# Kernel tuning notes

Measured on AMD Instinct MI355X. Metric: run time of the kernel, lower is better.

Reference implementation:

```python
import jax, jax.numpy as jnp
import numpy as np

DELTA = 0.1
B, U_DIM, D_DIM, H_DIM, Y_DIM = 4096, 256, 64, 8192, 256
ORDER = H_DIM // 2  # 2x2 rotation blocks


def setup_inputs() -> dict:
    key = jax.random.key(0)
    k = jax.random.split(key, 6)
    u = jax.random.normal(k[0], (B, U_DIM), jnp.float32)
    du = jax.random.normal(k[1], (B, D_DIM), jnp.float32)
    h = jax.random.normal(k[2], (1, H_DIM), jnp.float32)          # h_init state
    # torch.nn.init.uniform_ -> U[0,1); +0.05 keeps 1/omega well-conditioned
    omega = jax.random.uniform(k[3], (ORDER,), jnp.float32) + 0.05
    B_w = jax.random.normal(k[4], (H_DIM, U_DIM + D_DIM), jnp.float32) / np.sqrt(U_DIM + D_DIM)
    C_w = jax.random.normal(k[5], (Y_DIM, H_DIM), jnp.float32) / np.sqrt(H_DIM)
    return {"u": u, "du": du, "h": h, "omega": omega, "B_w": B_w, "C_w": C_w}


def reference(u, du, h, omega, B_w, C_w):
    cos_t = jnp.cos(omega * DELTA)   # [order]
    sin_t = jnp.sin(omega * DELTA)   # [order]
    # exact rotation of state pairs: h viewed as [*, order, 2]
    hp = h.reshape(-1, ORDER, 2)
    h1 = cos_t * hp[..., 0] + sin_t * hp[..., 1]
    h2 = -sin_t * hp[..., 0] + cos_t * hp[..., 1]
    rec = jnp.stack([h1, h2], axis=-1).reshape(h.shape[0], -1)    # [1, h_dim]
    # input projection u_hat = B([du, u])
    udu = jnp.concatenate([du, u], axis=1)                        # [B, d+u]
    u_hat = (udu @ B_w.T).reshape(-1, ORDER, 2)                   # [B, order, 2]
    cm1 = cos_t - 1.0
    inp1 = (sin_t * u_hat[..., 0] - cm1 * u_hat[..., 1]) / omega
    inp2 = (cm1 * u_hat[..., 0] + sin_t * u_hat[..., 1]) / omega
    inp = jnp.stack([inp1, inp2], axis=-1).reshape(udu.shape[0], -1)  # [B, h_dim]
    h_new = rec + inp                                             # broadcast [B, h_dim]
    # sigma = identity, C linear readout (no bias)
    y = h_new @ C_w.T                                             # [B, y_dim]
    return y
```

## Files before the change

### kernel.cpp

```cpp
#include <hip/hip_runtime.h>
#include <hip/hip_bf16.h>

#define BN    4096
#define U_DIM 256
#define D_DIM 64
#define H_DIM 8192
#define Y_DIM 256
#define C_DIM 320
#define DELTAF 0.1f

typedef __bf16 bf16_t;
typedef __attribute__((ext_vector_type(2))) bf16_t bf16x2;
typedef __attribute__((ext_vector_type(8))) bf16_t bf16x8;
typedef __attribute__((ext_vector_type(4))) float f32x4;

__global__ __launch_bounds__(256) void prep_ceff_y0(
    const float* __restrict__ Cw, const float* __restrict__ hin,
    const float* __restrict__ omega, bf16_t* __restrict__ Ceff,
    float* __restrict__ y0) {
  const int row = blockIdx.x;
  const int t = threadIdx.x;
  const float* crow = Cw + (size_t)row * H_DIM;
  bf16_t* erow = Ceff + (size_t)row * H_DIM;
  float acc = 0.f;
#pragma unroll
  for (int p = 0; p < 16; ++p) {
    const int j = p * 256 + t;
    const float om = omega[j];
    const float ang = om * DELTAF;
    const float s = __sinf(ang);
    const float c = __cosf(ang);
    const float cm1 = c - 1.0f;
    const float inv = 1.0f / om;
    const float2 cw = *(const float2*)(crow + 2 * j);
    const float e0 = (cw.x * s + cw.y * cm1) * inv;
    const float e1 = (cw.y * s - cw.x * cm1) * inv;
    bf16x2 ev;
    ev.x = (bf16_t)e0;
    ev.y = (bf16_t)e1;
    *(bf16x2*)(erow + 2 * j) = ev;
    const float2 hp = *(const float2*)(hin + 2 * j);
    const float r0 = c * hp.x + s * hp.y;
    const float r1 = c * hp.y - s * hp.x;
    acc += cw.x * r0 + cw.y * r1;
  }
#pragma unroll
  for (int off = 32; off > 0; off >>= 1) acc += __shfl_down(acc, off);
  __shared__ float red[4];
  if ((t & 63) == 0) red[t >> 6] = acc;
  __syncthreads();
  if (t == 0) y0[row] = red[0] + red[1] + red[2] + red[3];
}

__global__ __launch_bounds__(256) void prep_bt(const float* __restrict__ Bw,
                                               bf16_t* __restrict__ Bt) {
  __shared__ float tile[64][65];
  const int k0 = blockIdx.x * 64;
  const int n0 = blockIdx.y * 64;
  const int t = threadIdx.x;
#pragma unroll
  for (int i = 0; i < 4; ++i) {
    const int li = i * 256 + t;
    const int r = li >> 4;
    const int c4 = (li & 15) * 4;
    const float4 v = *(const float4*)(Bw + (size_t)(k0 + r) * C_DIM + n0 + c4);
    tile[r][c4 + 0] = v.x;
    tile[r][c4 + 1] = v.y;
    tile[r][c4 + 2] = v.z;
    tile[r][c4 + 3] = v.w;
  }
  __syncthreads();
#pragma unroll
  for (int i = 0; i < 2; ++i) {
    const int li = i * 256 + t;
    const int rn = li >> 3;
    const int ck = (li & 7) * 8;
    union {
      bf16_t h[8];
      int4 v;
    } o;
#pragma unroll
    for (int j = 0; j < 8; ++j) o.h[j] = (bf16_t)tile[ck + j][rn];
    *(int4*)(Bt + (size_t)(n0 + rn) * H_DIM + k0 + ck) = o.v;
  }
}

__global__ __launch_bounds__(256) void gemm_E(const bf16_t* __restrict__ Ceff,
                                              const bf16_t* __restrict__ Bt,
                                              float* __restrict__ E) {
  const int bm = blockIdx.x;
  const int bn = blockIdx.y;
  const int ks = blockIdx.z;
  const int t = threadIdx.x;
  const int wave = t >> 6, lane = t & 63;
  const int wm = wave >> 1, wn = wave & 1;
  const int l15 = lane & 15, quad = lane >> 4;

  __shared__ bf16_t lA[64][40];
  __shared__ bf16_t lB[64][40];

  const int sr = t >> 2;
  const int sk = (t & 3) * 8;

  const bf16_t* gA = Ceff + (size_t)(bm * 64 + sr) * H_DIM + sk;
  const bf16_t* gB = Bt + (size_t)(bn * 64 + sr) * H_DIM + sk;

  f32x4 acc[2][2] = {};
  const int kbeg = ks * 512;
#pragma unroll 1
  for (int kk = kbeg; kk < kbeg + 512; kk += 32) {
    const int4 va = *(const int4*)(gA + kk);
    const int4 vb = *(const int4*)(gB + kk);
    __syncthreads();
    *(int4*)&lA[sr][sk] = va;
    *(int4*)&lB[sr][sk] = vb;
    __syncthreads();
    const bf16x8 a0 = *(bf16x8*)&lA[wm * 32 + l15][quad * 8];
    const bf16x8 a1 = *(bf16x8*)&lA[wm * 32 + 16 + l15][quad * 8];
    const bf16x8 b0 = *(bf16x8*)&lB[wn * 32 + l15][quad * 8];
    const bf16x8 b1 = *(bf16x8*)&lB[wn * 32 + 16 + l15][quad * 8];
    acc[0][0] = __builtin_amdgcn_mfma_f32_16x16x32_bf16(a0, b0, acc[0][0], 0, 0, 0);
    acc[0][1] = __builtin_amdgcn_mfma_f32_16x16x32_bf16(a0, b1, acc[0][1], 0, 0, 0);
    acc[1][0] = __builtin_amdgcn_mfma_f32_16x16x32_bf16(a1, b0, acc[1][0], 0, 0, 0);
    acc[1][1] = __builtin_amdgcn_mfma_f32_16x16x32_bf16(a1, b1, acc[1][1], 0, 0, 0);
  }
#pragma unroll
  for (int mt = 0; mt < 2; ++mt)
#pragma unroll
    for (int nt = 0; nt < 2; ++nt) {
      const int col = bn * 64 + wn * 32 + nt * 16 + l15;
#pragma unroll
      for (int r = 0; r < 4; ++r) {
        const int row = bm * 64 + wm * 32 + mt * 16 + quad * 4 + r;
        atomicAdd(&E[row * C_DIM + col], acc[mt][nt][r]);
      }
    }
}

__global__ __launch_bounds__(256) void gemm_Y(
    const float* __restrict__ u, const float* __restrict__ du,
    const float* __restrict__ E, const float* __restrict__ y0,
    float* __restrict__ out) {
  const int bm = blockIdx.x;
  const int bn = blockIdx.y;
  const int t = threadIdx.x;
  const int wave = t >> 6, lane = t & 63;
  const int wm = wave >> 1, wn = wave & 1;
  const int l15 = lane & 15, quad = lane >> 4;

  __shared__ bf16_t lA[64][40];
  __shared__ bf16_t lB[64][40];

  const int sr = t >> 2;
  const int sk = (t & 3) * 8;

  f32x4 acc[2][2] = {};
#pragma unroll 1
  for (int kk = 0; kk < C_DIM; kk += 32) {
    const int col = kk + sk;
    float4 v0, v1;
    if (col < D_DIM) {
      const float* p = du + (size_t)(bm * 64 + sr) * D_DIM + col;
      v0 = *(const float4*)p;
      v1 = *(const float4*)(p + 4);
    } else {
      const float* p = u + (size_t)(bm * 64 + sr) * U_DIM + (col - D_DIM);
      v0 = *(const float4*)p;
      v1 = *(const float4*)(p + 4);
    }
    const float* pe = E + (size_t)(bn * 64 + sr) * C_DIM + col;
    const float4 e0 = *(const float4*)pe;
    const float4 e1 = *(const float4*)(pe + 4);
    union {
      bf16_t h[8];
      int4 v;
    } pa, pb;
    pa.h[0] = (bf16_t)v0.x; pa.h[1] = (bf16_t)v0.y;
    pa.h[2] = (bf16_t)v0.z; pa.h[3] = (bf16_t)v0.w;
    pa.h[4] = (bf16_t)v1.x; pa.h[5] = (bf16_t)v1.y;
    pa.h[6] = (bf16_t)v1.z; pa.h[7] = (bf16_t)v1.w;
    pb.h[0] = (bf16_t)e0.x; pb.h[1] = (bf16_t)e0.y;
    pb.h[2] = (bf16_t)e0.z; pb.h[3] = (bf16_t)e0.w;
    pb.h[4] = (bf16_t)e1.x; pb.h[5] = (bf16_t)e1.y;
    pb.h[6] = (bf16_t)e1.z; pb.h[7] = (bf16_t)e1.w;
    __syncthreads();
    *(int4*)&lA[sr][sk] = pa.v;
    *(int4*)&lB[sr][sk] = pb.v;
    __syncthreads();
    const bf16x8 a0 = *(bf16x8*)&lA[wm * 32 + l15][quad * 8];
    const bf16x8 a1 = *(bf16x8*)&lA[wm * 32 + 16 + l15][quad * 8];
    const bf16x8 b0 = *(bf16x8*)&lB[wn * 32 + l15][quad * 8];
    const bf16x8 b1 = *(bf16x8*)&lB[wn * 32 + 16 + l15][quad * 8];
    acc[0][0] = __builtin_amdgcn_mfma_f32_16x16x32_bf16(a0, b0, acc[0][0], 0, 0, 0);
    acc[0][1] = __builtin_amdgcn_mfma_f32_16x16x32_bf16(a0, b1, acc[0][1], 0, 0, 0);
    acc[1][0] = __builtin_amdgcn_mfma_f32_16x16x32_bf16(a1, b0, acc[1][0], 0, 0, 0);
    acc[1][1] = __builtin_amdgcn_mfma_f32_16x16x32_bf16(a1, b1, acc[1][1], 0, 0, 0);
  }
#pragma unroll
  for (int nt = 0; nt < 2; ++nt) {
    const int col = bn * 64 + wn * 32 + nt * 16 + l15;
    const float yc = y0[col];
#pragma unroll
    for (int mt = 0; mt < 2; ++mt) {
#pragma unroll
      for (int r = 0; r < 4; ++r) {
        const int row = bm * 64 + wm * 32 + mt * 16 + quad * 4 + r;
        out[(size_t)row * Y_DIM + col] = acc[mt][nt][r] + yc;
      }
    }
  }
}

extern "C" void kernel_launch(void* const* d_in, const int* in_sizes, int n_in,
                              void* d_out, int out_size, void* d_ws,
                              size_t ws_size, hipStream_t stream) {
  const float* u = (const float*)d_in[0];
  const float* du = (const float*)d_in[1];
  const float* hin = (const float*)d_in[2];
  const float* omega = (const float*)d_in[3];
  const float* Bw = (const float*)d_in[4];
  const float* Cw = (const float*)d_in[5];
  float* out = (float*)d_out;

  char* ws = (char*)d_ws;
  float* E = (float*)ws;
  float* y0 = (float*)(ws + 327680);
  bf16_t* Ceff = (bf16_t*)(ws + 328704);
  bf16_t* Bt = (bf16_t*)(ws + 328704 + 4194304);

  hipMemsetAsync(E, 0, (size_t)Y_DIM * C_DIM * sizeof(float), stream);
  prep_ceff_y0<<<Y_DIM, 256, 0, stream>>>(Cw, hin, omega, Ceff, y0);
  prep_bt<<<dim3(H_DIM / 64, C_DIM / 64), 256, 0, stream>>>(Bw, Bt);
  gemm_E<<<dim3(4, 5, 16), 256, 0, stream>>>(Ceff, Bt, E);
  gemm_Y<<<dim3(BN / 64, Y_DIM / 64), 256, 0, stream>>>(u, du, E, y0, out);
}
```

Measured before the change: 111.1 us.

## Fuse prep kernels, compute Ceff on the fly in gemm_E, prefetch loads

Merges the memset, the Ceff/y0 prep and the B transpose into a single prep kernel that also writes per-pair sin, cos-1 and 1/omega coefficient tables. gemm_E now reads fp32 Cw directly and applies the rotation scaling while staging into LDS, so the bf16 Ceff intermediate is never written to or read back from global memory. Both GEMM loops are fully unrolled with a register prefetch of the next K-slice to overlap global loads with MFMA work. This saves launches and a round trip of the Ceff intermediate, at the cost of gemm_E reading twice as many A bytes (fp32) plus the coefficient tables, and doing extra ALU work per tile.

```diff
diff --git a/kernel.cpp b/kernel.cpp
--- a/kernel.cpp
+++ b/kernel.cpp
@@ -7,57 +7,26 @@
 #define H_DIM 8192
 #define Y_DIM 256
 #define C_DIM 320
+#define ORDER 4096
 #define DELTAF 0.1f
 
 typedef __bf16 bf16_t;
-typedef __attribute__((ext_vector_type(2))) bf16_t bf16x2;
 typedef __attribute__((ext_vector_type(8))) bf16_t bf16x8;
 typedef __attribute__((ext_vector_type(4))) float f32x4;
 
-__global__ __launch_bounds__(256) void prep_ceff_y0(
-    const float* __restrict__ Cw, const float* __restrict__ hin,
-    const float* __restrict__ omega, bf16_t* __restrict__ Ceff,
-    float* __restrict__ y0) {
-  const int row = blockIdx.x;
+__global__ __launch_bounds__(256) void prep(
+    const float* __restrict__ Bw, const float* __restrict__ Cw,
+    const float* __restrict__ hin, const float* __restrict__ omega,
+    bf16_t* __restrict__ Bt, float* __restrict__ coefS,
+    float* __restrict__ coefC, float* __restrict__ coefI,
+    float* __restrict__ y0, float* __restrict__ E) {
+  __shared__ float tile[64][65];
+  __shared__ float red[4];
+  const int bx = blockIdx.x;
   const int t = threadIdx.x;
-  const float* crow = Cw + (size_t)row * H_DIM;
-  bf16_t* erow = Ceff + (size_t)row * H_DIM;
-  float acc = 0.f;
-#pragma unroll
-  for (int p = 0; p < 16; ++p) {
-    const int j = p * 256 + t;
-    const float om = omega[j];
-    const float ang = om * DELTAF;
-    const float s = __sinf(ang);
-    const float c = __cosf(ang);
-    const float cm1 = c - 1.0f;
-    const float inv = 1.0f / om;
-    const float2 cw = *(const float2*)(crow + 2 * j);
-    const float e0 = (cw.x * s + cw.y * cm1) * inv;
-    const float e1 = (cw.y * s - cw.x * cm1) * inv;
-    bf16x2 ev;
-    ev.x = (bf16_t)e0;
-    ev.y = (bf16_t)e1;
-    *(bf16x2*)(erow + 2 * j) = ev;
-    const float2 hp = *(const float2*)(hin + 2 * j);
-    const float r0 = c * hp.x + s * hp.y;
-    const float r1 = c * hp.y - s * hp.x;
-    acc += cw.x * r0 + cw.y * r1;
-  }
-#pragma unroll
-  for (int off = 32; off > 0; off >>= 1) acc += __shfl_down(acc, off);
-  __shared__ float red[4];
-  if ((t & 63) == 0) red[t >> 6] = acc;
-  __syncthreads();
-  if (t == 0) y0[row] = red[0] + red[1] + red[2] + red[3];
-}
-
-__global__ __launch_bounds__(256) void prep_bt(const float* __restrict__ Bw,
-                                               bf16_t* __restrict__ Bt) {
-  __shared__ float tile[64][65];
-  const int k0 = blockIdx.x * 64;
-  const int n0 = blockIdx.y * 64;
-  const int t = threadIdx.x;
+  const int k0 = (bx & 127) * 64;
+  const int n0 = (bx >> 7) * 64;
+
 #pragma unroll
   for (int i = 0; i < 4; ++i) {
     const int li = i * 256 + t;
@@ -83,11 +52,48 @@
     for (int j = 0; j < 8; ++j) o.h[j] = (bf16_t)tile[ck + j][rn];
     *(int4*)(Bt + (size_t)(n0 + rn) * H_DIM + k0 + ck) = o.v;
   }
-}
-
-__global__ __launch_bounds__(256) void gemm_E(const bf16_t* __restrict__ Ceff,
-                                              const bf16_t* __restrict__ Bt,
-                                              float* __restrict__ E) {
+
+  if (bx < 16) {
+    const int j = bx * 256 + t;
+    const float om = omega[j];
+    const float ang = om * DELTAF;
+    coefS[j] = __sinf(ang);
+    coefC[j] = __cosf(ang) - 1.0f;
+    coefI[j] = 1.0f / om;
+  }
+
+  if (bx < 256) {
+    const float* crow = Cw + (size_t)bx * H_DIM;
+    float acc = 0.f;
+#pragma unroll
+    for (int p = 0; p < 16; ++p) {
+      const int j = p * 256 + t;
+      const float om = omega[j];
+      const float ang = om * DELTAF;
+      const float s = __sinf(ang);
+      const float c = __cosf(ang);
+      const float2 cw = *(const float2*)(crow + 2 * j);
+      const float2 hp = *(const float2*)(hin + 2 * j);
+      const float r0 = c * hp.x + s * hp.y;
+      const float r1 = c * hp.y - s * hp.x;
+      acc += cw.x * r0 + cw.y * r1;
+    }
+#pragma unroll
+    for (int off = 32; off > 0; off >>= 1) acc += __shfl_down(acc, off);
+    if ((t & 63) == 0) red[t >> 6] = acc;
+    __syncthreads();
+    if (t == 0) y0[bx] = red[0] + red[1] + red[2] + red[3];
+    if (t < 80) {
+      float4 z = {0.f, 0.f, 0.f, 0.f};
+      *(float4*)(E + (size_t)bx * C_DIM + t * 4) = z;
+    }
+  }
+}
+
+__global__ __launch_bounds__(256) void gemm_E(
+    const float* __restrict__ Cw, const bf16_t* __restrict__ Bt,
+    const float* __restrict__ coefS, const float* __restrict__ coefC,
+    const float* __restrict__ coefI, float* __restrict__ E) {
   const int bm = blockIdx.x;
   const int bn = blockIdx.y;
   const int ks = blockIdx.z;
@@ -101,19 +107,46 @@
 
   const int sr = t >> 2;
   const int sk = (t & 3) * 8;
-
-  const bf16_t* gA = Ceff + (size_t)(bm * 64 + sr) * H_DIM + sk;
+  const float* gA = Cw + (size_t)(bm * 64 + sr) * H_DIM + sk;
   const bf16_t* gB = Bt + (size_t)(bn * 64 + sr) * H_DIM + sk;
+
+  float4 va0, va1, cs, cc, ci;
+  int4 vb;
+  auto gload = [&](int kk) {
+    const float* p = gA + kk;
+    va0 = *(const float4*)p;
+    va1 = *(const float4*)(p + 4);
+    vb = *(const int4*)(gB + kk);
+    const int jp = (kk + sk) >> 1;
+    cs = *(const float4*)(coefS + jp);
+    cc = *(const float4*)(coefC + jp);
+    ci = *(const float4*)(coefI + jp);
+  };
+  auto stage = [&]() {
+    union {
+      bf16_t h[8];
+      int4 v;
+    } pa;
+    pa.h[0] = (bf16_t)((va0.x * cs.x + va0.y * cc.x) * ci.x);
+    pa.h[1] = (bf16_t)((va0.y * cs.x - va0.x * cc.x) * ci.x);
+    pa.h[2] = (bf16_t)((va0.z * cs.y + va0.w * cc.y) * ci.y);
+    pa.h[3] = (bf16_t)((va0.w * cs.y - va0.z * cc.y) * ci.y);
+    pa.h[4] = (bf16_t)((va1.x * cs.z + va1.y * cc.z) * ci.z);
+    pa.h[5] = (bf16_t)((va1.y * cs.z - va1.x * cc.z) * ci.z);
+    pa.h[6] = (bf16_t)((va1.z * cs.w + va1.w * cc.w) * ci.w);
+    pa.h[7] = (bf16_t)((va1.w * cs.w - va1.z * cc.w) * ci.w);
+    *(int4*)&lA[sr][sk] = pa.v;
+    *(int4*)&lB[sr][sk] = vb;
+  };
 
   f32x4 acc[2][2] = {};
   const int kbeg = ks * 512;
-#pragma unroll 1
-  for (int kk = kbeg; kk < kbeg + 512; kk += 32) {
-    const int4 va = *(const int4*)(gA + kk);
-    const int4 vb = *(const int4*)(gB + kk);
-    __syncthreads();
-    *(int4*)&lA[sr][sk] = va;
-    *(int4*)&lB[sr][sk] = vb;
+  gload(kbeg);
+#pragma unroll
+  for (int i = 0; i < 16; ++i) {
+    __syncthreads();
+    stage();
+    if (i < 15) gload(kbeg + (i + 1) * 32);
     __syncthreads();
     const bf16x8 a0 = *(bf16x8*)&lA[wm * 32 + l15][quad * 8];
     const bf16x8 a1 = *(bf16x8*)&lA[wm * 32 + 16 + l15][quad * 8];
@@ -154,11 +187,9 @@
   const int sr = t >> 2;
   const int sk = (t & 3) * 8;
 
-  f32x4 acc[2][2] = {};
-#pragma unroll 1
-  for (int kk = 0; kk < C_DIM; kk += 32) {
+  float4 v0, v1, e0, e1;
+  auto gload = [&](int kk) {
     const int col = kk + sk;
-    float4 v0, v1;
     if (col < D_DIM) {
       const float* p = du + (size_t)(bm * 64 + sr) * D_DIM + col;
       v0 = *(const float4*)p;
@@ -169,8 +200,10 @@
       v1 = *(const float4*)(p + 4);
     }
     const float* pe = E + (size_t)(bn * 64 + sr) * C_DIM + col;
-    const float4 e0 = *(const float4*)pe;
-    const float4 e1 = *(const float4*)(pe + 4);
+    e0 = *(const float4*)pe;
+    e1 = *(const float4*)(pe + 4);
+  };
+  auto stage = [&]() {
     union {
       bf16_t h[8];
       int4 v;
@@ -183,9 +216,17 @@
     pb.h[2] = (bf16_t)e0.z; pb.h[3] = (bf16_t)e0.w;
     pb.h[4] = (bf16_t)e1.x; pb.h[5] = (bf16_t)e1.y;
     pb.h[6] = (bf16_t)e1.z; pb.h[7] = (bf16_t)e1.w;
-    __syncthreads();
     *(int4*)&lA[sr][sk] = pa.v;
     *(int4*)&lB[sr][sk] = pb.v;
+  };
+
+  f32x4 acc[2][2] = {};
+  gload(0);
+#pragma unroll
+  for (int i = 0; i < 10; ++i) {
+    __syncthreads();
+    stage();
+    if (i < 9) gload((i + 1) * 32);
     __syncthreads();
     const bf16x8 a0 = *(bf16x8*)&lA[wm * 32 + l15][quad * 8];
     const bf16x8 a1 = *(bf16x8*)&lA[wm * 32 + 16 + l15][quad * 8];
@@ -225,12 +266,13 @@
   char* ws = (char*)d_ws;
   float* E = (float*)ws;
   float* y0 = (float*)(ws + 327680);
-  bf16_t* Ceff = (bf16_t*)(ws + 328704);
-  bf16_t* Bt = (bf16_t*)(ws + 328704 + 4194304);
-
-  hipMemsetAsync(E, 0, (size_t)Y_DIM * C_DIM * sizeof(float), stream);
-  prep_ceff_y0<<<Y_DIM, 256, 0, stream>>>(Cw, hin, omega, Ceff, y0);
-  prep_bt<<<dim3(H_DIM / 64, C_DIM / 64), 256, 0, stream>>>(Bw, Bt);
-  gemm_E<<<dim3(4, 5, 16), 256, 0, stream>>>(Ceff, Bt, E);
+  float* coefS = (float*)(ws + 328704);
+  float* coefC = (float*)(ws + 345088);
+  float* coefI = (float*)(ws + 361472);
+  bf16_t* Bt = (bf16_t*)(ws + 377856);
+
+  prep<<<640, 256, 0, stream>>>(Bw, Cw, hin, omega, Bt, coefS, coefC, coefI,
+                                y0, E);
+  gemm_E<<<dim3(4, 5, 16), 256, 0, stream>>>(Cw, Bt, coefS, coefC, coefI, E);
   gemm_Y<<<dim3(BN / 64, Y_DIM / 64), 256, 0, stream>>>(u, du, E, y0, out);
 }
```

Result: faster. 97.48 us (-12.3%).
